# Optimization experiments

Hardware: AMD Instinct MI355X
Metric: run time of the kernel (lower is better)

Reference implementation:

```python
import jax, jax.numpy as jnp
import numpy as np

# Config (DiffWave-style)
C = 64        # channels
K = 3         # kernel_size
L = 30        # num_layers
CYCLES = 3    # num_cycles
DRATE = 2     # dilation_rate
ITER = 50     # diffusion steps
ESIZE = 128   # embedding_size
EPROJ = 512   # embedding_proj
EFACT = 4.0   # embedding_factor
B, T = 4, 16384
LAYERS_PER_CYCLE = L // CYCLES
DILATIONS = [DRATE ** (i % LAYERS_PER_CYCLE) for i in range(L)]
INV_SQRT2 = 1.0 / np.sqrt(2.0).astype(np.float32)


def _embed_table():
    # [ITER, ESIZE] sinusoidal noise-schedule embedding (deterministic buffer)
    logit = jnp.linspace(0.0, 1.0, ESIZE // 2)
    exp = jnp.power(10.0, logit * EFACT)
    t = jnp.arange(1, ITER + 1, dtype=jnp.float32)
    comp = exp[None, :] * t[:, None]
    return jnp.concatenate([jnp.sin(comp), jnp.cos(comp)], axis=-1)


def _dconv(x, w, d):
    # x: [B,T,Cin], w: [K,Cin,Cout], SAME padding, dilation d -> [B,T,Cout]
    return jax.lax.conv_general_dilated(
        x, w, window_strides=(1,), padding='SAME', rhs_dilation=(d,),
        dimension_numbers=('NWC', 'WIO', 'NWC'))


def setup_inputs() -> dict:
    key = jax.random.key(0)
    ks = jax.random.split(key, 20)
    g = lambda k, shape, fan_in: (jax.random.normal(k, shape) / np.sqrt(fan_in)).astype(jnp.float32)
    return {
        'signal': jax.random.normal(ks[0], (B, T), dtype=jnp.float32),
        'timestep': jax.random.randint(ks[1], (B,), 1, ITER + 1, dtype=jnp.int32),
        'in_w': g(ks[2], (1, C), 1),
        'in_b': jnp.zeros((C,), jnp.float32),
        'pe0_w': g(ks[3], (ESIZE, EPROJ), ESIZE),
        'pe0_b': jnp.zeros((EPROJ,), jnp.float32),
        'pe1_w': g(ks[4], (EPROJ, EPROJ), EPROJ),
        'pe1_b': jnp.zeros((EPROJ,), jnp.float32),
        'blk_emb_w': g(ks[5], (L, EPROJ, C), EPROJ),
        'blk_emb_b': jnp.zeros((L, C), jnp.float32),
        'blk_conv_w': g(ks[6], (L, K, C, 2 * C), K * C),
        'blk_conv_b': jnp.zeros((L, 2 * C), jnp.float32),
        'blk_res_w': g(ks[7], (L - 1, C, C), C),
        'blk_res_b': jnp.zeros((L - 1, C), jnp.float32),
        'blk_skip_w': g(ks[8], (L, C, C), C),
        'blk_skip_b': jnp.zeros((L, C), jnp.float32),
        'out0_w': g(ks[9], (C, C), C),
        'out0_b': jnp.zeros((C,), jnp.float32),
        'out1_w': g(ks[10], (C, 1), C),
        'out1_b': jnp.zeros((1,), jnp.float32),
    }


def reference(signal, timestep, in_w, in_b, pe0_w, pe0_b, pe1_w, pe1_b,
              blk_emb_w, blk_emb_b, blk_conv_w, blk_conv_b,
              blk_res_w, blk_res_b, blk_skip_w, blk_skip_b,
              out0_w, out0_b, out1_w, out1_b):
    # input 1x1 conv + relu: [B,T] -> [B,T,C]
    x = jax.nn.relu(signal[..., None] * in_w[0][None, None, :] + in_b)
    # noise-schedule embedding [B,ESIZE] -> swish MLP -> [B,EPROJ]
    embed = _embed_table()[timestep - 1]
    embed = jax.nn.swish(embed @ pe0_w + pe0_b)
    embed = jax.nn.swish(embed @ pe1_w + pe1_b)
    skip_sum = jnp.zeros_like(x)
    for i in range(L):
        e = embed @ blk_emb_w[i] + blk_emb_b[i]           # [B,C]
        h = x + e[:, None, :]                              # [B,T,C]
        y = _dconv(h, blk_conv_w[i], DILATIONS[i]) + blk_conv_b[i]  # [B,T,2C]
        z = jnp.tanh(y[..., :C]) * jax.nn.sigmoid(y[..., C:])       # gated
        if i < L - 1:
            x = (z @ blk_res_w[i] + blk_res_b[i] + x) * INV_SQRT2
        skip_sum = skip_sum + (z @ blk_skip_w[i] + blk_skip_b[i])
    ctx = skip_sum / np.sqrt(L).astype(np.float32)
    ctx = jax.nn.relu(ctx @ out0_w + out0_b)
    out = ctx @ out1_w + out1_b                            # [B,T,1]
    return jnp.squeeze(out, axis=-1)
```

## Files before the change

### kernel.cpp

```cpp
#include <hip/hip_runtime.h>
#include <math.h>

#define TT 16384
#define BB 4
#define CC 64
#define LL 30

typedef _Float16 f16;
typedef _Float16 f16x4 __attribute__((ext_vector_type(4)));
typedef _Float16 f16x8 __attribute__((ext_vector_type(8)));
typedef float f32x4 __attribute__((ext_vector_type(4)));
typedef unsigned int u32;

#define MFMA(a, b, c) __builtin_amdgcn_mfma_f32_16x16x32_f16(a, b, c, 0, 0, 0)

__device__ __forceinline__ float fsig(float x) { return 1.0f / (1.0f + __expf(-x)); }
__device__ __forceinline__ float ftanhf(float x) { return 1.0f - 2.0f / (__expf(2.0f * x) + 1.0f); }

__device__ __forceinline__ void gl_lds16(const void* g, void* l) {
    __builtin_amdgcn_global_load_lds((const __attribute__((address_space(1))) u32*)g,
                                     (__attribute__((address_space(3))) u32*)l, 16, 0, 0);
}

__global__ void pack_weights(const float* __restrict__ conv_w, const float* __restrict__ res_w,
                             const float* __restrict__ skip_w, const float* __restrict__ out0_w,
                             f16* __restrict__ wcv, f16* __restrict__ wrs, f16* __restrict__ wsk,
                             f16* __restrict__ wo0) {
    const int total_c = LL * 6 * 8 * 64 * 8;
    const int total_r = (LL - 1) * 2 * 4 * 64 * 8;
    const int total_s = LL * 2 * 4 * 64 * 8;
    const int total_o = 2 * 4 * 64 * 8;
    const int total = total_c + total_r + total_s + total_o;
    for (int i = blockIdx.x * blockDim.x + threadIdx.x; i < total; i += gridDim.x * blockDim.x) {
        if (i < total_c) {
            int e = i & 7, lane = (i >> 3) & 63, mf = (i >> 9) & 7, rest = i >> 12;
            int ks = rest % 6, l = rest / 6;
            int cin = (ks & 1) * 32 + (lane >> 4) * 8 + e;
            int tap = ks >> 1;
            int cout = mf * 16 + (lane & 15);
            wcv[i] = (f16)conv_w[(((size_t)l * 3 + tap) * 64 + cin) * 128 + cout];
        } else if (i < total_c + total_r) {
            int j = i - total_c;
            int e = j & 7, lane = (j >> 3) & 63, mf = (j >> 9) & 3, kk = (j >> 11) & 1, l = j >> 12;
            int cin = kk * 32 + (lane >> 4) * 8 + e;
            int cout = mf * 16 + (lane & 15);
            wrs[j] = (f16)res_w[((size_t)l * 64 + cin) * 64 + cout];
        } else if (i < total_c + total_r + total_s) {
            int j = i - total_c - total_r;
            int e = j & 7, lane = (j >> 3) & 63, mf = (j >> 9) & 3, kk = (j >> 11) & 1, l = j >> 12;
            int cin = kk * 32 + (lane >> 4) * 8 + e;
            int cout = mf * 16 + (lane & 15);
            wsk[j] = (f16)skip_w[((size_t)l * 64 + cin) * 64 + cout];
        } else {
            int j = i - total_c - total_r - total_s;
            int e = j & 7, lane = (j >> 3) & 63, mf = (j >> 9) & 3, kk = (j >> 11) & 1;
            int cin = kk * 32 + (lane >> 4) * 8 + e;
            int c = mf * 16 + (lane & 15);
            wo0[j] = (f16)out0_w[cin * 64 + c];
        }
    }
}

__global__ void init_x_kernel(const float* __restrict__ signal, const float* __restrict__ in_w,
                              const float* __restrict__ in_b, f16* __restrict__ x0) {
    int i = blockIdx.x * 256 + threadIdx.x;
    int bt = i >> 3, g = i & 7;
    float s = signal[bt];
    f32x4 w0 = *(const f32x4*)&in_w[g * 8];
    f32x4 w1 = *(const f32x4*)&in_w[g * 8 + 4];
    f32x4 b0 = *(const f32x4*)&in_b[g * 8];
    f32x4 b1 = *(const f32x4*)&in_b[g * 8 + 4];
    f16x8 o;
#pragma unroll
    for (int j = 0; j < 4; ++j) {
        o[j] = (f16)fmaxf(s * w0[j] + b0[j], 0.f);
        o[4 + j] = (f16)fmaxf(s * w1[j] + b1[j], 0.f);
    }
    *(f16x8*)&x0[(size_t)bt * CC + g * 8] = o;
}

__global__ void embed_stage1(const int* __restrict__ timestep, const float* __restrict__ pe0_w,
                             const float* __restrict__ pe0_b, float* __restrict__ h1) {
    __shared__ float emb[BB * 128];
    const int tid = threadIdx.x;
    for (int i = tid; i < BB * 128; i += 256) {
        int b = i >> 7, j = i & 127, jj = j & 63;
        float logit = (jj == 63) ? 1.0f : (float)jj * (1.0f / 63.0f);
        double e10 = pow(10.0, (double)(4.0f * logit));
        float comp = (float)e10 * (float)timestep[b];
        emb[i] = (j < 64) ? (float)sin((double)comp) : (float)cos((double)comp);
    }
    __syncthreads();
    const int col = blockIdx.x * 64 + (tid & 63), b = tid >> 6;
    float s = 0.f;
    for (int j = 0; j < 128; ++j) s += emb[b * 128 + j] * pe0_w[j * 512 + col];
    s += pe0_b[col];
    h1[b * 512 + col] = s * fsig(s);
}

__global__ void embed_stage2(const float* __restrict__ h1, const float* __restrict__ pe1_w,
                             const float* __restrict__ pe1_b, float* __restrict__ embed2) {
    __shared__ float hs[BB * 512];
    const int tid = threadIdx.x;
    for (int i = tid; i < BB * 512; i += 256) hs[i] = h1[i];
    __syncthreads();
    const int col = blockIdx.x * 64 + (tid & 63), b = tid >> 6;
    float s = 0.f;
    for (int j = 0; j < 512; ++j) s += hs[b * 512 + j] * pe1_w[j * 512 + col];
    s += pe1_b[col];
    embed2[b * 512 + col] = s * fsig(s);
}

__global__ void e_kernel(const float* __restrict__ embed2, const float* __restrict__ blk_emb_w,
                         const float* __restrict__ blk_emb_b, float* __restrict__ e_out) {
    const int l = blockIdx.x, b = blockIdx.y;
    const int tid = threadIdx.x;
    __shared__ float em[512];
    __shared__ float red[256];
    for (int i = tid; i < 512; i += 256) em[i] = embed2[b * 512 + i];
    __syncthreads();
    const int c = tid & 63, part = tid >> 6;
    float s0 = 0.f, s1 = 0.f;
    for (int j = part * 128; j < part * 128 + 128; j += 2) {
        s0 += em[j] * blk_emb_w[((size_t)l * 512 + j) * 64 + c];
        s1 += em[j + 1] * blk_emb_w[((size_t)l * 512 + j + 1) * 64 + c];
    }
    red[tid] = s0 + s1;
    __syncthreads();
    if (tid < 64)
        e_out[(l * BB + b) * 64 + tid] =
            red[tid] + red[tid + 64] + red[tid + 128] + red[tid + 192] + blk_emb_b[l * 64 + tid];
}

__global__ void evec2_kernel(const float* __restrict__ e_in, const float* __restrict__ conv_w,
                             const float* __restrict__ conv_b, float* __restrict__ evec) {
    const int l = blockIdx.x, tap = blockIdx.y, b = blockIdx.z;
    const int n = threadIdx.x;
    __shared__ float es[64];
    if (n < 64) es[n] = e_in[(l * BB + b) * 64 + n];
    __syncthreads();
    const float* cw = conv_w + ((size_t)(l * 3 + tap) * 64) * 128;
    float a0 = 0.f, a1 = 0.f, a2 = 0.f, a3 = 0.f;
#pragma unroll
    for (int k = 0; k < 64; k += 4) {
        a0 += es[k] * cw[k * 128 + n];
        a1 += es[k + 1] * cw[(k + 1) * 128 + n];
        a2 += es[k + 2] * cw[(k + 2) * 128 + n];
        a3 += es[k + 3] * cw[(k + 3) * 128 + n];
    }
    float s = a0 + a1 + a2 + a3 + ((tap == 1) ? conv_b[l * 128 + n] : 0.f);
    evec[((size_t)(l * 4 + b) * 3 + tap) * 128 + n] = s;
}

__global__ void sbsum_kernel(const float* __restrict__ skip_b, float* __restrict__ sbsum) {
    int c = threadIdx.x;
    float s = 0.f;
    for (int l = 0; l < LL; ++l) s += skip_b[l * 64 + c];
    sbsum[c] = s;
}

__launch_bounds__(256)
__global__ void layer_kernel(const f16* __restrict__ xin, f16* __restrict__ xout,
                             f16* __restrict__ zg,
                             const f16* __restrict__ wcv, const f16* __restrict__ wrs,
                             const float* __restrict__ evec_l, const float* __restrict__ res_b,
                             const f16* __restrict__ zpage, int d) {
    extern __shared__ f16 lds[];
    const int tid = threadIdx.x, lane = tid & 63, w = tid >> 6;
    const int lrow = lane & 15, lk = lane >> 4;
    const int b = blockIdx.y, t0 = blockIdx.x * 64;
    const int stride = (d < 64) ? d : 64;
    const int R8 = (64 + 2 * stride + 7) & ~7;
    f16* xs = lds;
    f16* zs = lds + R8 * 64;
    const f16* xb = xin + (size_t)b * TT * CC;
    f16* zb = zg + (size_t)b * TT * CC;

    const int NCH = R8 >> 3;
    for (int chunk = w; chunk < NCH; chunk += 4) {
        int gid = chunk * 64 + lane;
        int r = gid >> 3, g = gid & 7;
        int t = t0 - d + r + ((d > 64) ? ((r >> 6) * (d - 64)) : 0);
        const f16* src = ((unsigned)t < TT) ? (xb + (size_t)t * CC + ((g ^ (r & 7)) << 3)) : zpage;
        gl_lds16(src, (void*)((char*)xs + chunk * 1024));
    }
    __syncthreads();

    f32x4 acc[2][4] = {};
#pragma unroll
    for (int ks = 0; ks < 6; ++ks) {
        const int tap = ks >> 1, kk = ks & 1;
        f16x8 aw0 = *(const f16x8*)&wcv[((ks * 8 + w) * 64 + lane) * 8];
        f16x8 aw1 = *(const f16x8*)&wcv[((ks * 8 + w + 4) * 64 + lane) * 8];
#pragma unroll
        for (int nfi = 0; nfi < 4; ++nfi) {
            int r = nfi * 16 + lrow + tap * stride;
            int g = kk * 4 + lk;
            f16x8 bx = *(const f16x8*)&xs[r * 64 + ((g ^ (r & 7)) << 3)];
            acc[0][nfi] = MFMA(aw0, bx, acc[0][nfi]);
            acc[1][nfi] = MFMA(aw1, bx, acc[1][nfi]);
        }
    }

    const float* evb = evec_l + b * 384;
    const int ca = w * 16 + lk * 4;
    const int gz = ca >> 3;
    f32x4 e0a = *(const f32x4*)&evb[ca], e1a = *(const f32x4*)&evb[128 + ca],
          e2a = *(const f32x4*)&evb[256 + ca];
    f32x4 e0b = *(const f32x4*)&evb[64 + ca], e1b = *(const f32x4*)&evb[192 + ca],
          e2b = *(const f32x4*)&evb[320 + ca];
#pragma unroll
    for (int nfi = 0; nfi < 4; ++nfi) {
        int trow = nfi * 16 + lrow;
        int t = t0 + trow;
        float m0 = (t >= d) ? 1.f : 0.f;
        float m2 = (t + d < TT) ? 1.f : 0.f;
        f16x4 zo;
#pragma unroll
        for (int r = 0; r < 4; ++r) {
            float ya = acc[0][nfi][r] + e1a[r] + m0 * e0a[r] + m2 * e2a[r];
            float yb = acc[1][nfi][r] + e1b[r] + m0 * e0b[r] + m2 * e2b[r];
            zo[r] = (f16)(ftanhf(ya) * fsig(yb));
        }
        *(f16x4*)&zs[trow * 64 + ((gz ^ (trow & 7)) << 3) + (ca & 7)] = zo;
        *(f16x4*)&zb[(size_t)(t0 + trow) * CC + ca] = zo;
    }

    if (wrs != nullptr) {
        __syncthreads();
        f32x4 accR[4] = {};
#pragma unroll
        for (int kk = 0; kk < 2; ++kk) {
            f16x8 ar_ = *(const f16x8*)&wrs[((kk * 4 + w) * 64 + lane) * 8];
#pragma unroll
            for (int nfi = 0; nfi < 4; ++nfi) {
                int trow = nfi * 16 + lrow;
                int g = kk * 4 + lk;
                f16x8 bz = *(const f16x8*)&zs[trow * 64 + ((g ^ (trow & 7)) << 3)];
                accR[nfi] = MFMA(ar_, bz, accR[nfi]);
            }
        }
        f16* xob = xout + (size_t)b * TT * CC;
        f32x4 rb4 = *(const f32x4*)&res_b[ca];
#pragma unroll
        for (int nfi = 0; nfi < 4; ++nfi) {
            int trow = nfi * 16 + lrow;
            int rr = stride + trow;
            f16x4 xv = *(const f16x4*)&xs[rr * 64 + ((gz ^ (rr & 7)) << 3) + (ca & 7)];
            f16x4 xo;
#pragma unroll
            for (int r = 0; r < 4; ++r)
                xo[r] = (f16)((accR[nfi][r] + rb4[r] + (float)xv[r]) * 0.70710678118654752f);
            *(f16x4*)&xob[(size_t)(t0 + trow) * CC + ca] = xo;
        }
    }
}

__launch_bounds__(256)
__global__ void skip_head(const f16* __restrict__ zbuf, const f16* __restrict__ z29,
                          const f16* __restrict__ wsk, const f16* __restrict__ wo0,
                          const float* __restrict__ sbsum, const float* __restrict__ out0_b,
                          const float* __restrict__ out1_w, const float* __restrict__ out1_b,
                          float* __restrict__ out) {
    __shared__ f16 zb[2][64 * 64];
    const int tid = threadIdx.x, lane = tid & 63, w = tid >> 6;
    const int lrow = lane & 15, lk = lane >> 4;
    const int lin = blockIdx.x;
    const int lin2 = (lin & 7) * 128 + (lin >> 3);
    const int b = lin2 >> 8, tile = lin2 & 255;
    const int t0 = tile * 64;

#define STAGE_Z(L, BUF)                                                                       \
    {                                                                                         \
        const f16* zl =                                                                       \
            (((L) < LL - 1) ? (zbuf + (size_t)(L)*BB * TT * CC) : z29) + (size_t)b * TT * CC; \
        _Pragma("unroll") for (int j = 0; j < 2; ++j) {                                       \
            int chunk = j * 4 + w;                                                            \
            int gid = chunk * 64 + lane;                                                      \
            int r = gid >> 3, g = gid & 7;                                                    \
            gl_lds16(zl + (size_t)(t0 + r) * CC + ((g ^ (r & 7)) << 3),                       \
                     (void*)((char*)zb[BUF] + chunk * 1024));                                 \
        }                                                                                     \
    }

    f32x4 accS[4] = {};
    STAGE_Z(0, 0);
    for (int l = 0; l < LL; ++l) {
        __syncthreads();
        if (l + 1 < LL) STAGE_Z(l + 1, (l + 1) & 1);
        const f16* wl = wsk + (size_t)l * 4096;
        const f16* zcur = zb[l & 1];
#pragma unroll
        for (int kk = 0; kk < 2; ++kk) {
            f16x8 as_ = *(const f16x8*)&wl[((kk * 4 + w) * 64 + lane) * 8];
#pragma unroll
            for (int nt = 0; nt < 4; ++nt) {
                int trow = nt * 16 + lrow;
                int g = kk * 4 + lk;
                f16x8 bz = *(const f16x8*)&zcur[trow * 64 + ((g ^ (trow & 7)) << 3)];
                accS[nt] = MFMA(as_, bz, accS[nt]);
            }
        }
    }

    __syncthreads();
    const float invL = 0.18257418583505537f;
    const int cb = w * 16 + lk * 4;
    const int gz = cb >> 3;
    f32x4 sb4 = *(const f32x4*)&sbsum[cb];
#pragma unroll
    for (int nt = 0; nt < 4; ++nt) {
        int row = nt * 16 + lrow;
        f16x4 sn;
#pragma unroll
        for (int r = 0; r < 4; ++r) sn[r] = (f16)((accS[nt][r] + sb4[r]) * invL);
        *(f16x4*)&zb[0][row * 64 + ((gz ^ (row & 7)) << 3) + (cb & 7)] = sn;
    }
    __syncthreads();

    const int trow = w * 16 + lrow;
    f32x4 accO[4] = {};
#pragma unroll
    for (int kk = 0; kk < 2; ++kk) {
        int g = kk * 4 + lk;
        f16x8 bz = *(const f16x8*)&zb[0][trow * 64 + ((g ^ (trow & 7)) << 3)];
#pragma unroll
        for (int mf = 0; mf < 4; ++mf) {
            f16x8 aw = *(const f16x8*)&wo0[((kk * 4 + mf) * 64 + lane) * 8];
            accO[mf] = MFMA(aw, bz, accO[mf]);
        }
    }
    float pv = 0.f;
    const float b1 = out1_b[0];
#pragma unroll
    for (int mf = 0; mf < 4; ++mf) {
        int c = mf * 16 + lk * 4;
        f32x4 b0 = *(const f32x4*)&out0_b[c];
        f32x4 w1 = *(const f32x4*)&out1_w[c];
#pragma unroll
        for (int r = 0; r < 4; ++r) pv += fmaxf(accO[mf][r] + b0[r], 0.f) * w1[r];
    }
    pv += __shfl_xor(pv, 16);
    pv += __shfl_xor(pv, 32);
    if (lane < 16) out[(size_t)b * TT + t0 + w * 16 + lane] = pv + b1;
#undef STAGE_Z
}

extern "C" void kernel_launch(void* const* d_in, const int* in_sizes, int n_in,
                              void* d_out, int out_size, void* d_ws, size_t ws_size,
                              hipStream_t stream) {
    const float* signal = (const float*)d_in[0];
    const int* timestep = (const int*)d_in[1];
    const float* in_w = (const float*)d_in[2];
    const float* in_b = (const float*)d_in[3];
    const float* pe0_w = (const float*)d_in[4];
    const float* pe0_b = (const float*)d_in[5];
    const float* pe1_w = (const float*)d_in[6];
    const float* pe1_b = (const float*)d_in[7];
    const float* blk_emb_w = (const float*)d_in[8];
    const float* blk_emb_b = (const float*)d_in[9];
    const float* blk_conv_w = (const float*)d_in[10];
    const float* blk_conv_b = (const float*)d_in[11];
    const float* blk_res_w = (const float*)d_in[12];
    const float* blk_res_b = (const float*)d_in[13];
    const float* blk_skip_w = (const float*)d_in[14];
    const float* blk_skip_b = (const float*)d_in[15];
    const float* out0_w = (const float*)d_in[16];
    const float* out0_b = (const float*)d_in[17];
    const float* out1_w = (const float*)d_in[18];
    const float* out1_b = (const float*)d_in[19];

    char* p = (char*)d_ws;
    const size_t xhsz = (size_t)BB * TT * CC * sizeof(f16);
    const size_t BTC = (size_t)BB * TT * CC;
    f16* xa = (f16*)p; p += xhsz;
    f16* xb2 = (f16*)p; p += xhsz;
    f16* wcv = (f16*)p; p += (size_t)737280 * 2;
    f16* wrs = (f16*)p; p += (size_t)118784 * 2;
    f16* wsk = (f16*)p; p += (size_t)122880 * 2;
    f16* wo0 = (f16*)p; p += (size_t)4096 * 2;
    float* h1 = (float*)p; p += 4 * 512 * sizeof(float);
    float* embed2 = (float*)p; p += 4 * 512 * sizeof(float);
    float* e_buf = (float*)p; p += (size_t)LL * BB * 64 * sizeof(float);
    float* evec = (float*)p; p += (size_t)LL * 4 * 3 * 128 * sizeof(float);
    float* sbsum = (float*)p; p += 64 * sizeof(float);
    f16* zpage = (f16*)p; p += 256;
    p = (char*)(((size_t)p + 255) & ~(size_t)255);
    f16* zbuf = (f16*)p; p += (size_t)(LL - 1) * xhsz;

    hipMemsetAsync(zpage, 0, 256, stream);
    pack_weights<<<1024, 256, 0, stream>>>(blk_conv_w, blk_res_w, blk_skip_w, out0_w,
                                           wcv, wrs, wsk, wo0);
    init_x_kernel<<<2048, 256, 0, stream>>>(signal, in_w, in_b, xa);
    embed_stage1<<<8, 256, 0, stream>>>(timestep, pe0_w, pe0_b, h1);
    embed_stage2<<<8, 256, 0, stream>>>(h1, pe1_w, pe1_b, embed2);
    e_kernel<<<dim3(LL, BB), 256, 0, stream>>>(embed2, blk_emb_w, blk_emb_b, e_buf);
    evec2_kernel<<<dim3(LL, 3, BB), 128, 0, stream>>>(e_buf, blk_conv_w, blk_conv_b, evec);
    sbsum_kernel<<<1, 64, 0, stream>>>(blk_skip_b, sbsum);

    f16* cur = xa;
    f16* nxt = xb2;
    f16* z29 = xa;
    for (int i = 0; i < LL; ++i) {
        int d = 1 << (i % 10);
        bool last = (i == LL - 1);
        f16* zg = last ? nxt : (zbuf + (size_t)i * BTC);
        if (last) z29 = nxt;
        int stride = (d < 64) ? d : 64;
        int R8 = (64 + 2 * stride + 7) & ~7;
        size_t smem = (size_t)(R8 * 64 + 64 * 64) * sizeof(f16);
        layer_kernel<<<dim3(TT / 64, BB), 256, smem, stream>>>(
            cur, nxt, zg, wcv + (size_t)i * 24576,
            last ? nullptr : (wrs + (size_t)i * 4096), evec + (size_t)i * 1536,
            last ? nullptr : (blk_res_b + i * 64), zpage, d);
        if (!last) { f16* t = cur; cur = nxt; nxt = t; }
    }

    skip_head<<<(BB * TT) / 64, 256, 0, stream>>>(zbuf, z29, wsk, wo0, sbsum, out0_b, out1_w,
                                                  out1_b, (float*)d_out);
}
```

Before: 541.3 us.

## Fuse per-layer skip projection into layer kernel, reduce skip sums in head

Each layer kernel now applies that layer's skip 1x1 projection to the gated activations while they are still in LDS, and stores the fp16 skip output instead of the raw gate output. The skip_head kernel no longer runs 30 MFMA projections. It only sums the 30 stored skip tensors elementwise, then applies the output MLP on 32-row tiles. This moves MFMA work into kernels that already hold z in LDS and makes the head a plain streaming reduction. The cost is rounding each per-layer skip output to fp16 before summation, which adds precision risk, while global traffic stays about the same.

```diff
diff --git a/kernel.cpp b/kernel.cpp
--- a/kernel.cpp
+++ b/kernel.cpp
@@ -161,8 +161,9 @@
 
 __launch_bounds__(256)
 __global__ void layer_kernel(const f16* __restrict__ xin, f16* __restrict__ xout,
-                             f16* __restrict__ zg,
+                             f16* __restrict__ sg,
                              const f16* __restrict__ wcv, const f16* __restrict__ wrs,
+                             const f16* __restrict__ wsk,
                              const float* __restrict__ evec_l, const float* __restrict__ res_b,
                              const f16* __restrict__ zpage, int d) {
     extern __shared__ f16 lds[];
@@ -174,7 +175,7 @@
     f16* xs = lds;
     f16* zs = lds + R8 * 64;
     const f16* xb = xin + (size_t)b * TT * CC;
-    f16* zb = zg + (size_t)b * TT * CC;
+    f16* sb = sg + (size_t)b * TT * CC;
 
     const int NCH = R8 >> 3;
     for (int chunk = w; chunk < NCH; chunk += 4) {
@@ -223,28 +224,36 @@
             zo[r] = (f16)(ftanhf(ya) * fsig(yb));
         }
         *(f16x4*)&zs[trow * 64 + ((gz ^ (trow & 7)) << 3) + (ca & 7)] = zo;
-        *(f16x4*)&zb[(size_t)(t0 + trow) * CC + ca] = zo;
-    }
-
-    if (wrs != nullptr) {
-        __syncthreads();
-        f32x4 accR[4] = {};
-#pragma unroll
-        for (int kk = 0; kk < 2; ++kk) {
-            f16x8 ar_ = *(const f16x8*)&wrs[((kk * 4 + w) * 64 + lane) * 8];
-#pragma unroll
-            for (int nfi = 0; nfi < 4; ++nfi) {
-                int trow = nfi * 16 + lrow;
-                int g = kk * 4 + lk;
-                f16x8 bz = *(const f16x8*)&zs[trow * 64 + ((g ^ (trow & 7)) << 3)];
-                accR[nfi] = MFMA(ar_, bz, accR[nfi]);
-            }
-        }
-        f16* xob = xout + (size_t)b * TT * CC;
-        f32x4 rb4 = *(const f32x4*)&res_b[ca];
+    }
+    __syncthreads();
+
+    const bool has_res = (wrs != nullptr);
+    f32x4 accR[4] = {}, accS[4] = {};
+#pragma unroll
+    for (int kk = 0; kk < 2; ++kk) {
+        f16x8 as_ = *(const f16x8*)&wsk[((kk * 4 + w) * 64 + lane) * 8];
+        f16x8 ar_ = {};
+        if (has_res) ar_ = *(const f16x8*)&wrs[((kk * 4 + w) * 64 + lane) * 8];
 #pragma unroll
         for (int nfi = 0; nfi < 4; ++nfi) {
             int trow = nfi * 16 + lrow;
+            int g = kk * 4 + lk;
+            f16x8 bz = *(const f16x8*)&zs[trow * 64 + ((g ^ (trow & 7)) << 3)];
+            accS[nfi] = MFMA(as_, bz, accS[nfi]);
+            if (has_res) accR[nfi] = MFMA(ar_, bz, accR[nfi]);
+        }
+    }
+
+    f16* xob = has_res ? (xout + (size_t)b * TT * CC) : nullptr;
+    f32x4 rb4 = has_res ? *(const f32x4*)&res_b[ca] : f32x4{0.f, 0.f, 0.f, 0.f};
+#pragma unroll
+    for (int nfi = 0; nfi < 4; ++nfi) {
+        int trow = nfi * 16 + lrow;
+        f16x4 so;
+#pragma unroll
+        for (int r = 0; r < 4; ++r) so[r] = (f16)accS[nfi][r];
+        *(f16x4*)&sb[(size_t)(t0 + trow) * CC + ca] = so;
+        if (has_res) {
             int rr = stride + trow;
             f16x4 xv = *(const f16x4*)&xs[rr * 64 + ((gz ^ (rr & 7)) << 3) + (ca & 7)];
             f16x4 xo;
@@ -257,93 +266,70 @@
 }
 
 __launch_bounds__(256)
-__global__ void skip_head(const f16* __restrict__ zbuf, const f16* __restrict__ z29,
-                          const f16* __restrict__ wsk, const f16* __restrict__ wo0,
-                          const float* __restrict__ sbsum, const float* __restrict__ out0_b,
-                          const float* __restrict__ out1_w, const float* __restrict__ out1_b,
-                          float* __restrict__ out) {
-    __shared__ f16 zb[2][64 * 64];
+__global__ void skip_head(const f16* __restrict__ sbuf, const f16* __restrict__ s29,
+                          const f16* __restrict__ wo0, const float* __restrict__ sbsum,
+                          const float* __restrict__ out0_b, const float* __restrict__ out1_w,
+                          const float* __restrict__ out1_b, float* __restrict__ out) {
+    __shared__ f16 sn[32 * 64];
     const int tid = threadIdx.x, lane = tid & 63, w = tid >> 6;
     const int lrow = lane & 15, lk = lane >> 4;
     const int lin = blockIdx.x;
-    const int lin2 = (lin & 7) * 128 + (lin >> 3);
-    const int b = lin2 >> 8, tile = lin2 & 255;
-    const int t0 = tile * 64;
-
-#define STAGE_Z(L, BUF)                                                                       \
-    {                                                                                         \
-        const f16* zl =                                                                       \
-            (((L) < LL - 1) ? (zbuf + (size_t)(L)*BB * TT * CC) : z29) + (size_t)b * TT * CC; \
-        _Pragma("unroll") for (int j = 0; j < 2; ++j) {                                       \
-            int chunk = j * 4 + w;                                                            \
-            int gid = chunk * 64 + lane;                                                      \
-            int r = gid >> 3, g = gid & 7;                                                    \
-            gl_lds16(zl + (size_t)(t0 + r) * CC + ((g ^ (r & 7)) << 3),                       \
-                     (void*)((char*)zb[BUF] + chunk * 1024));                                 \
-        }                                                                                     \
-    }
-
-    f32x4 accS[4] = {};
-    STAGE_Z(0, 0);
+    const int lin2 = (lin & 7) * 256 + (lin >> 3);
+    const int b = lin2 >> 9, tile = lin2 & 511;
+    const int t0 = tile * 32;
+    const int row = tid >> 3, ch8 = tid & 7;
+
+    const size_t base = ((size_t)b * TT + t0 + row) * CC + ch8 * 8;
+    f32x4 a0 = {}, a1 = {};
+#pragma unroll
     for (int l = 0; l < LL; ++l) {
-        __syncthreads();
-        if (l + 1 < LL) STAGE_Z(l + 1, (l + 1) & 1);
-        const f16* wl = wsk + (size_t)l * 4096;
-        const f16* zcur = zb[l & 1];
+        const f16* sl = (l < LL - 1) ? (sbuf + (size_t)l * BB * TT * CC) : s29;
+        f16x8 v = *(const f16x8*)&sl[base];
+#pragma unroll
+        for (int r = 0; r < 4; ++r) {
+            a0[r] += (float)v[r];
+            a1[r] += (float)v[4 + r];
+        }
+    }
+    const float invL = 0.18257418583505537f;
+    f32x4 sb0 = *(const f32x4*)&sbsum[ch8 * 8];
+    f32x4 sb1 = *(const f32x4*)&sbsum[ch8 * 8 + 4];
+    f16x8 o;
+#pragma unroll
+    for (int r = 0; r < 4; ++r) {
+        o[r] = (f16)((a0[r] + sb0[r]) * invL);
+        o[4 + r] = (f16)((a1[r] + sb1[r]) * invL);
+    }
+    *(f16x8*)&sn[row * 64 + ((ch8 ^ (row & 7)) << 3)] = o;
+    __syncthreads();
+
+    if (w < 2) {
+        const int trow = w * 16 + lrow;
+        f32x4 accO[4] = {};
 #pragma unroll
         for (int kk = 0; kk < 2; ++kk) {
-            f16x8 as_ = *(const f16x8*)&wl[((kk * 4 + w) * 64 + lane) * 8];
-#pragma unroll
-            for (int nt = 0; nt < 4; ++nt) {
-                int trow = nt * 16 + lrow;
-                int g = kk * 4 + lk;
-                f16x8 bz = *(const f16x8*)&zcur[trow * 64 + ((g ^ (trow & 7)) << 3)];
-                accS[nt] = MFMA(as_, bz, accS[nt]);
+            int g = kk * 4 + lk;
+            f16x8 bz = *(const f16x8*)&sn[trow * 64 + ((g ^ (trow & 7)) << 3)];
+#pragma unroll
+            for (int mf = 0; mf < 4; ++mf) {
+                f16x8 aw = *(const f16x8*)&wo0[((kk * 4 + mf) * 64 + lane) * 8];
+                accO[mf] = MFMA(aw, bz, accO[mf]);
             }
         }
-    }
-
-    __syncthreads();
-    const float invL = 0.18257418583505537f;
-    const int cb = w * 16 + lk * 4;
-    const int gz = cb >> 3;
-    f32x4 sb4 = *(const f32x4*)&sbsum[cb];
-#pragma unroll
-    for (int nt = 0; nt < 4; ++nt) {
-        int row = nt * 16 + lrow;
-        f16x4 sn;
-#pragma unroll
-        for (int r = 0; r < 4; ++r) sn[r] = (f16)((accS[nt][r] + sb4[r]) * invL);
-        *(f16x4*)&zb[0][row * 64 + ((gz ^ (row & 7)) << 3) + (cb & 7)] = sn;
-    }
-    __syncthreads();
-
-    const int trow = w * 16 + lrow;
-    f32x4 accO[4] = {};
-#pragma unroll
-    for (int kk = 0; kk < 2; ++kk) {
-        int g = kk * 4 + lk;
-        f16x8 bz = *(const f16x8*)&zb[0][trow * 64 + ((g ^ (trow & 7)) << 3)];
+        float pv = 0.f;
+        const float b1 = out1_b[0];
 #pragma unroll
         for (int mf = 0; mf < 4; ++mf) {
-            f16x8 aw = *(const f16x8*)&wo0[((kk * 4 + mf) * 64 + lane) * 8];
-            accO[mf] = MFMA(aw, bz, accO[mf]);
-        }
-    }
-    float pv = 0.f;
-    const float b1 = out1_b[0];
-#pragma unroll
-    for (int mf = 0; mf < 4; ++mf) {
-        int c = mf * 16 + lk * 4;
-        f32x4 b0 = *(const f32x4*)&out0_b[c];
-        f32x4 w1 = *(const f32x4*)&out1_w[c];
-#pragma unroll
-        for (int r = 0; r < 4; ++r) pv += fmaxf(accO[mf][r] + b0[r], 0.f) * w1[r];
-    }
-    pv += __shfl_xor(pv, 16);
-    pv += __shfl_xor(pv, 32);
-    if (lane < 16) out[(size_t)b * TT + t0 + w * 16 + lane] = pv + b1;
-#undef STAGE_Z
+            int c = mf * 16 + lk * 4;
+            f32x4 b0 = *(const f32x4*)&out0_b[c];
+            f32x4 w1 = *(const f32x4*)&out1_w[c];
+#pragma unroll
+            for (int r = 0; r < 4; ++r) pv += fmaxf(accO[mf][r] + b0[r], 0.f) * w1[r];
+        }
+        pv += __shfl_xor(pv, 16);
+        pv += __shfl_xor(pv, 32);
+        if (lane < 16) out[(size_t)b * TT + t0 + w * 16 + lane] = pv + b1;
+    }
 }
 
 extern "C" void kernel_launch(void* const* d_in, const int* in_sizes, int n_in,
@@ -386,7 +372,7 @@
     float* sbsum = (float*)p; p += 64 * sizeof(float);
     f16* zpage = (f16*)p; p += 256;
     p = (char*)(((size_t)p + 255) & ~(size_t)255);
-    f16* zbuf = (f16*)p; p += (size_t)(LL - 1) * xhsz;
+    f16* sbuf = (f16*)p; p += (size_t)(LL - 1) * xhsz;
 
     hipMemsetAsync(zpage, 0, 256, stream);
     pack_weights<<<1024, 256, 0, stream>>>(blk_conv_w, blk_res_w, blk_skip_w, out0_w,
@@ -400,22 +386,23 @@
 
     f16* cur = xa;
     f16* nxt = xb2;
-    f16* z29 = xa;
+    f16* s29 = xa;
     for (int i = 0; i < LL; ++i) {
         int d = 1 << (i % 10);
         bool last = (i == LL - 1);
-        f16* zg = last ? nxt : (zbuf + (size_t)i * BTC);
-        if (last) z29 = nxt;
+        f16* sg = last ? nxt : (sbuf + (size_t)i * BTC);
+        if (last) s29 = nxt;
         int stride = (d < 64) ? d : 64;
         int R8 = (64 + 2 * stride + 7) & ~7;
         size_t smem = (size_t)(R8 * 64 + 64 * 64) * sizeof(f16);
         layer_kernel<<<dim3(TT / 64, BB), 256, smem, stream>>>(
-            cur, nxt, zg, wcv + (size_t)i * 24576,
-            last ? nullptr : (wrs + (size_t)i * 4096), evec + (size_t)i * 1536,
+            cur, nxt, sg, wcv + (size_t)i * 24576,
+            last ? nullptr : (wrs + (size_t)i * 4096),
+            wsk + (size_t)i * 4096, evec + (size_t)i * 1536,
             last ? nullptr : (blk_res_b + i * 64), zpage, d);
         if (!last) { f16* t = cur; cur = nxt; nxt = t; }
     }
 
-    skip_head<<<(BB * TT) / 64, 256, 0, stream>>>(zbuf, z29, wsk, wo0, sbsum, out0_b, out1_w,
+    skip_head<<<(BB * TT) / 32, 256, 0, stream>>>(sbuf, s29, wo0, sbsum, out0_b, out1_w,
                                                   out1_b, (float*)d_out);
 }
```

New measurement: 618.4 us. 1.14x slower.
